# Kernel tuning notes

Hardware: AMD Instinct MI355X
Metric: run time of the kernel (lower is better)

The kernel has to match this reference:

```python
import jax, jax.numpy as jnp
import numpy as np

B, C, H, W = 32, 256, 64, 64
h, w = 8, 8          # partition size
S = 4                # num_sharesets
RED = 4              # globalperceptron_reduce
EPS = 1e-5           # BatchNorm eps


def setup_inputs() -> dict:
    key = jax.random.key(0)
    ks = jax.random.split(key, 20)
    Ci = C // RED
    def bn_params(i):
        return (1.0 + 0.1 * jax.random.normal(ks[i], (S,), jnp.float32),      # gamma
                0.1 * jax.random.normal(ks[i + 1], (S,), jnp.float32),        # beta
                0.1 * jax.random.normal(ks[i + 2], (S,), jnp.float32),        # running_mean
                jax.random.uniform(ks[i + 3], (S,), jnp.float32, 0.5, 1.5))   # running_var
    g3, b3, m3, v3 = bn_params(6)
    g1, b1, m1, v1 = bn_params(10)
    gk, bk, mk, vk = bn_params(14)
    return {
        "x": jax.random.normal(ks[0], (B, C, H, W), jnp.float32),
        # GlobalPerceptron (1x1 convs on pooled vector == dense layers)
        "fc1_w": 0.05 * jax.random.normal(ks[1], (Ci, C), jnp.float32),
        "fc1_b": jnp.zeros((Ci,), jnp.float32),
        "fc2_w": 0.05 * jax.random.normal(ks[2], (C, Ci), jnp.float32),
        "fc2_b": jnp.zeros((C,), jnp.float32),
        # fc3: grouped 1x1 conv over S*h*w channels -> S independent (h*w,h*w) mats
        "fc3_w": 0.05 * jax.random.normal(ks[3], (S, h * w, h * w), jnp.float32),
        "fc3bn_g": g3, "fc3bn_b": b3, "fc3bn_m": m3, "fc3bn_v": v3,
        # reparam depthwise conv branches (k=1 and k=3), groups=S
        "conv1_w": 0.1 * jax.random.normal(ks[4], (S, 1, 1, 1), jnp.float32),
        "bn1_g": g1, "bn1_b": b1, "bn1_m": m1, "bn1_v": v1,
        "conv3_w": 0.1 * jax.random.normal(ks[5], (S, 1, 3, 3), jnp.float32),
        "bn3_g": gk, "bn3_b": bk, "bn3_m": mk, "bn3_v": vk,
    }


def _bn(x, g, b, m, v):
    # inference-mode BatchNorm2d over channel dim 1 (S channels)
    scale = g / jnp.sqrt(v + EPS)
    return x * scale[None, :, None, None] + (b - m * scale)[None, :, None, None]


def _dwconv(x, wgt, k):
    # depthwise (groups=S) conv, stride 1, SAME-ish padding k//2
    return jax.lax.conv_general_dilated(
        x, wgt, (1, 1), [(k // 2, k // 2)] * 2,
        feature_group_count=S, dimension_numbers=("NCHW", "OIHW", "NCHW"))


def reference(x, fc1_w, fc1_b, fc2_w, fc2_b, fc3_w,
              fc3bn_g, fc3bn_b, fc3bn_m, fc3bn_v,
              conv1_w, bn1_g, bn1_b, bn1_m, bn1_v,
              conv3_w, bn3_g, bn3_b, bn3_m, bn3_v):
    hp, wp = H // h, W // w
    # GlobalPerceptron gate: avgpool -> fc -> relu -> fc -> sigmoid
    pooled = x.mean((2, 3))  # (B, C)
    gate = jax.nn.sigmoid(jnp.maximum(pooled @ fc1_w.T + fc1_b, 0.0) @ fc2_w.T + fc2_b)
    # partition: (B,C,H,W) -> (B,hp,wp,C,h,w)
    parts = x.reshape(B, C, hp, h, wp, w).transpose(0, 2, 4, 1, 3, 5)
    # fc3 grouped 1x1 conv: rows of S consecutive channels' (h*w) patches
    fc_in = parts.reshape(-1, S, h * w)                      # (B*hp*wp*C/S, S, h*w)
    fc3_out = jnp.einsum('nsi,soi->nso', fc_in, fc3_w).reshape(-1, S, h, w)
    fc3_out = _bn(fc3_out, fc3bn_g, fc3bn_b, fc3bn_m, fc3bn_v)
    # multi-branch depthwise convs on the same partitions, summed
    conv_in = parts.reshape(-1, S, h, w)
    conv_out = (_bn(_dwconv(conv_in, conv1_w, 1), bn1_g, bn1_b, bn1_m, bn1_v)
                + _bn(_dwconv(conv_in, conv3_w, 3), bn3_g, bn3_b, bn3_m, bn3_v))
    # merge, un-partition (literal translation of the torch reshape/permute chain)
    out = (fc3_out + conv_out).reshape(-1, hp, wp, S, h, w)
    out = out.transpose(0, 3, 1, 4, 2, 5).reshape(B, C, H, W)
    return out * gate[:, :, None, None]
```

## Files before the change

### kernel.cpp

```cpp
#include <hip/hip_runtime.h>
#include <hip/hip_bf16.h>
#include <math.h>

#define BN_EPS 1e-5f

typedef __attribute__((ext_vector_type(8))) short short8;
typedef __attribute__((ext_vector_type(4))) float f32x4;

__device__ __forceinline__ unsigned short bfbits(float f) {
  __hip_bfloat16 h = __float2bfloat16(f);
  return *reinterpret_cast<unsigned short*>(&h);
}
__device__ __forceinline__ float bf2f(unsigned short u) {
  union { unsigned v; float f; } c; c.v = ((unsigned)u) << 16;
  return c.f;
}

__global__ __launch_bounds__(256) void prep_pool_kernel(
    const float* __restrict__ x, float* __restrict__ pooled,
    const float* __restrict__ fc3_w,
    const float* __restrict__ g3, const float* __restrict__ b3,
    const float* __restrict__ m3, const float* __restrict__ v3,
    const float* __restrict__ c1w,
    const float* __restrict__ g1, const float* __restrict__ b1,
    const float* __restrict__ m1, const float* __restrict__ v1,
    const float* __restrict__ c3w,
    const float* __restrict__ gk, const float* __restrict__ bk,
    const float* __restrict__ mk, const float* __restrict__ vk,
    unsigned short* __restrict__ ahi, unsigned short* __restrict__ alo,
    float* __restrict__ totb) {
  int bid = blockIdx.x;
  int tid = threadIdx.x;
  if (bid < 16) {
    int s = bid >> 2;
    int o = (bid & 3) * 16 + (tid >> 4);
    int kc = (tid & 15) * 4;
    float sc3 = g3[s] * rsqrtf(v3[s] + BN_EPS);
    float sc1 = g1[s] * rsqrtf(v1[s] + BN_EPS);
    float sck = gk[s] * rsqrtf(vk[s] + BN_EPS);
    float c0 = sc1 * c1w[s] + sck * c3w[s * 9 + 4];
    int oh = o >> 3, ow = o & 7;
    unsigned short H[4], L[4];
#pragma unroll
    for (int j = 0; j < 4; ++j) {
      int k = kc + j;
      int kh = k >> 3, kw = k & 7;
      float a = sc3 * fc3_w[(s * 64 + o) * 64 + k];
      int dy = kh - oh, dx = kw - ow;
      if (dy >= -1 && dy <= 1 && dx >= -1 && dx <= 1)
        a += (dy == 0 && dx == 0) ? c0 : sck * c3w[s * 9 + (dy + 1) * 3 + (dx + 1)];
      unsigned short h = bfbits(a);
      H[j] = h;
      L[j] = bfbits(a - bf2f(h));
    }
    size_t base = (size_t)(s * 64 + o) * 64 + kc;
    *(ushort4*)(ahi + base) = make_ushort4(H[0], H[1], H[2], H[3]);
    *(ushort4*)(alo + base) = make_ushort4(L[0], L[1], L[2], L[3]);
    if (bid == 0 && tid < 4) {
      int ss = tid;
      float s3 = g3[ss] * rsqrtf(v3[ss] + BN_EPS);
      float s1 = g1[ss] * rsqrtf(v1[ss] + BN_EPS);
      float sk = gk[ss] * rsqrtf(vk[ss] + BN_EPS);
      totb[ss] = (b3[ss] - m3[ss] * s3) + (b1[ss] - m1[ss] * s1) + (bk[ss] - mk[ss] * sk);
    }
    return;
  }
  int w = tid >> 6, lane = tid & 63;
  int bc = (bid - 16) * 4 + w;
  const f32x4* xp = (const f32x4*)(x + (size_t)bc * 4096);
  float ssum = 0.f;
#pragma unroll
  for (int i = 0; i < 16; ++i) {
    f32x4 v = xp[i * 64 + lane];
    ssum += (v.x + v.y) + (v.z + v.w);
  }
#pragma unroll
  for (int m = 32; m >= 1; m >>= 1) ssum += __shfl_xor(ssum, m, 64);
  if (lane == 0) pooled[bc] = ssum * (1.f / 4096.f);
}

__global__ __launch_bounds__(256) void gate_kernel(const float* __restrict__ pooled,
                                                   const float* __restrict__ fc1_w,
                                                   const float* __restrict__ fc1_b,
                                                   const float* __restrict__ fc2_w,
                                                   const float* __restrict__ fc2_b,
                                                   float* __restrict__ gate) {
  int b = blockIdx.x;
  int tid = threadIdx.x;
  __shared__ float p[256];
  __shared__ float hbuf[64];
  p[tid] = pooled[b * 256 + tid];
  __syncthreads();
  if (tid < 64) {
    float a = fc1_b[tid];
    const float* wr = fc1_w + tid * 256;
#pragma unroll 8
    for (int c = 0; c < 256; ++c) a += p[c] * wr[c];
    hbuf[tid] = fmaxf(a, 0.f);
  }
  __syncthreads();
  float g = fc2_b[tid];
  const float* w2 = fc2_w + tid * 64;
#pragma unroll 8
  for (int j = 0; j < 64; ++j) g += hbuf[j] * w2[j];
  gate[b * 256 + tid] = 1.f / (1.f + expf(-g));
}

__global__ __launch_bounds__(512, 4) void main_kernel(
    const float* __restrict__ x,
    const unsigned short* __restrict__ ahi, const unsigned short* __restrict__ alo,
    const float* __restrict__ totb, const float* __restrict__ gate,
    float* __restrict__ out) {
  __shared__ unsigned short xs[33280];

  int bid = blockIdx.x;
  int cgh = bid & 7;
  int hpi = (bid >> 3) & 7;
  int b   = bid >> 6;
  int tid = threadIdx.x;
  int wv  = tid >> 6;
  int s    = __builtin_amdgcn_readfirstlane(wv & 3);
  int half = __builtin_amdgcn_readfirstlane(wv >> 2);
  int r16 = tid & 15;
  int g   = (tid >> 4) & 3;

  f32x4 gbuf[8];
#pragma unroll
  for (int i = 0; i < 8; ++i) {
    int flat = i * 512 + tid;
    int slot = flat >> 7;
    int off  = flat & 127;
    int row  = off >> 4, w4 = off & 15;
    int c = cgh * 32 + (slot & 7) * 4 + (slot >> 3);
    gbuf[i] = *(const f32x4*)(x + (size_t)(b * 256 + c) * 4096 + (hpi * 8 + row) * 64 + w4 * 4);
  }

  short8 Ah[2][2], Al[2][2];
#pragma unroll
  for (int oti = 0; oti < 2; ++oti)
#pragma unroll
    for (int kt = 0; kt < 2; ++kt) {
      size_t off = (size_t)(s * 64 + (half * 2 + oti) * 16 + r16) * 64 + kt * 32 + g * 8;
      Ah[kt][oti] = *(const short8*)(ahi + off);
      Al[kt][oti] = *(const short8*)(alo + off);
    }
  float gmul[4];
#pragma unroll
  for (int nt = 0; nt < 4; ++nt)
    gmul[nt] = gate[b * 256 + hpi * 32 + (nt * 2 + (r16 >> 3)) * 4 + s];
  float tb = totb[s];

#pragma unroll
  for (int i = 0; i < 8; ++i) {
    int flat = i * 512 + tid;
    int slot = flat >> 7;
    int off  = flat & 127;
    int row  = off >> 4, w4 = off & 15;
    float fv[4] = {gbuf[i].x, gbuf[i].y, gbuf[i].z, gbuf[i].w};
    ushort4 H, L;
    unsigned short h0 = bfbits(fv[0]), h1 = bfbits(fv[1]), h2 = bfbits(fv[2]), h3 = bfbits(fv[3]);
    H = make_ushort4(h0, h1, h2, h3);
    L = make_ushort4(bfbits(fv[0] - bf2f(h0)), bfbits(fv[1] - bf2f(h1)),
                     bfbits(fv[2] - bf2f(h2)), bfbits(fv[3] - bf2f(h3)));
    int base = slot * 520 + row * 64 + w4 * 4;
    *(ushort4*)&xs[base] = H;
    *(ushort4*)&xs[16640 + base] = L;
  }

  __syncthreads();

  f32x4 acc[2][4];
#pragma unroll
  for (int i = 0; i < 2; ++i)
#pragma unroll
    for (int j = 0; j < 4; ++j) acc[i][j] = f32x4{0.f, 0.f, 0.f, 0.f};

  int jch = r16 & 7;
#pragma unroll
  for (int kt = 0; kt < 2; ++kt)
#pragma unroll
    for (int nt = 0; nt < 4; ++nt) {
      int wpi = nt * 2 + (r16 >> 3);
      int addr = (s * 8 + jch) * 520 + (kt * 4 + g) * 64 + wpi * 8;
      short8 BH = *(const short8*)&xs[addr];
      short8 BL = *(const short8*)&xs[16640 + addr];
#pragma unroll
      for (int oti = 0; oti < 2; ++oti) {
        acc[oti][nt] = __builtin_amdgcn_mfma_f32_16x16x32_bf16(Ah[kt][oti], BH, acc[oti][nt], 0, 0, 0);
        acc[oti][nt] = __builtin_amdgcn_mfma_f32_16x16x32_bf16(Ah[kt][oti], BL, acc[oti][nt], 0, 0, 0);
        acc[oti][nt] = __builtin_amdgcn_mfma_f32_16x16x32_bf16(Al[kt][oti], BH, acc[oti][nt], 0, 0, 0);
      }
    }

#pragma unroll
  for (int nt = 0; nt < 4; ++nt) {
    int n2 = nt * 16 + r16;
    int c_out = hpi * 32 + (n2 >> 3) * 4 + s;
    float gm = gmul[nt];
    float* outb = out + (size_t)(b * 256 + c_out) * 4096 + cgh * 8 * 64 + (n2 & 7) * 8;
#pragma unroll
    for (int oti = 0; oti < 2; ++oti) {
      f32x4 a = acc[oti][nt];
      int hh = (half * 2 + oti) * 2 + (g >> 1);
      int wo = (g & 1) * 4;
      f32x4 o4 = {(a.x + tb) * gm, (a.y + tb) * gm,
                  (a.z + tb) * gm, (a.w + tb) * gm};
      __builtin_nontemporal_store(o4, (f32x4*)(outb + hh * 64 + wo));
    }
  }
}

extern "C" void kernel_launch(void* const* d_in, const int* in_sizes, int n_in,
                              void* d_out, int out_size, void* d_ws, size_t ws_size,
                              hipStream_t stream) {
  const float* x     = (const float*)d_in[0];
  const float* fc1_w = (const float*)d_in[1];
  const float* fc1_b = (const float*)d_in[2];
  const float* fc2_w = (const float*)d_in[3];
  const float* fc2_b = (const float*)d_in[4];
  const float* fc3_w = (const float*)d_in[5];
  const float* g3  = (const float*)d_in[6];
  const float* b3  = (const float*)d_in[7];
  const float* m3  = (const float*)d_in[8];
  const float* v3  = (const float*)d_in[9];
  const float* c1w = (const float*)d_in[10];
  const float* g1  = (const float*)d_in[11];
  const float* b1  = (const float*)d_in[12];
  const float* m1  = (const float*)d_in[13];
  const float* v1  = (const float*)d_in[14];
  const float* c3w = (const float*)d_in[15];
  const float* gk  = (const float*)d_in[16];
  const float* bk  = (const float*)d_in[17];
  const float* mk  = (const float*)d_in[18];
  const float* vk  = (const float*)d_in[19];
  float* out = (float*)d_out;

  float* pooled = (float*)d_ws;
  float* gate   = pooled + 8192;
  unsigned short* ahi = (unsigned short*)(gate + 8192);
  unsigned short* alo = ahi + 16384;
  float* totb   = (float*)(alo + 16384);

  prep_pool_kernel<<<2064, 256, 0, stream>>>(x, pooled, fc3_w, g3, b3, m3, v3,
                                             c1w, g1, b1, m1, v1, c3w, gk, bk,
                                             mk, vk, ahi, alo, totb);
  gate_kernel<<<32, 256, 0, stream>>>(pooled, fc1_w, fc1_b, fc2_w, fc2_b, gate);
  main_kernel<<<2048, 512, 0, stream>>>(x, ahi, alo, totb, gate, out);
}
```

Baseline: 75.20 us.

## Fuse gate MLP into main kernel and reverse block order

```diff
diff --git a/kernel.cpp b/kernel.cpp
--- a/kernel.cpp
+++ b/kernel.cpp
@@ -79,46 +79,25 @@
   if (lane == 0) pooled[bc] = ssum * (1.f / 4096.f);
 }
 
-__global__ __launch_bounds__(256) void gate_kernel(const float* __restrict__ pooled,
-                                                   const float* __restrict__ fc1_w,
-                                                   const float* __restrict__ fc1_b,
-                                                   const float* __restrict__ fc2_w,
-                                                   const float* __restrict__ fc2_b,
-                                                   float* __restrict__ gate) {
-  int b = blockIdx.x;
-  int tid = threadIdx.x;
-  __shared__ float p[256];
-  __shared__ float hbuf[64];
-  p[tid] = pooled[b * 256 + tid];
-  __syncthreads();
-  if (tid < 64) {
-    float a = fc1_b[tid];
-    const float* wr = fc1_w + tid * 256;
-#pragma unroll 8
-    for (int c = 0; c < 256; ++c) a += p[c] * wr[c];
-    hbuf[tid] = fmaxf(a, 0.f);
-  }
-  __syncthreads();
-  float g = fc2_b[tid];
-  const float* w2 = fc2_w + tid * 64;
-#pragma unroll 8
-  for (int j = 0; j < 64; ++j) g += hbuf[j] * w2[j];
-  gate[b * 256 + tid] = 1.f / (1.f + expf(-g));
-}
-
 __global__ __launch_bounds__(512, 4) void main_kernel(
     const float* __restrict__ x,
     const unsigned short* __restrict__ ahi, const unsigned short* __restrict__ alo,
-    const float* __restrict__ totb, const float* __restrict__ gate,
+    const float* __restrict__ totb, const float* __restrict__ pooled,
+    const float* __restrict__ fc1_w, const float* __restrict__ fc1_b,
+    const float* __restrict__ fc2_w, const float* __restrict__ fc2_b,
     float* __restrict__ out) {
   __shared__ unsigned short xs[33280];
-
-  int bid = blockIdx.x;
+  __shared__ float partL[512];
+  __shared__ float hidL[64];
+  __shared__ float gmulL[32];
+
+  int bid = 2047 - (int)blockIdx.x;
   int cgh = bid & 7;
   int hpi = (bid >> 3) & 7;
   int b   = bid >> 6;
   int tid = threadIdx.x;
   int wv  = tid >> 6;
+  int lane = tid & 63;
   int s    = __builtin_amdgcn_readfirstlane(wv & 3);
   int half = __builtin_amdgcn_readfirstlane(wv >> 2);
   int r16 = tid & 15;
@@ -135,6 +114,21 @@
     gbuf[i] = *(const f32x4*)(x + (size_t)(b * 256 + c) * 4096 + (hpi * 8 + row) * 64 + w4 * 4);
   }
 
+  {
+    int h = wv * 8 + (lane >> 3);
+    int k = lane & 7;
+    const float* fw = fc1_w + h * 256 + k * 32;
+    const float* pp = pooled + b * 256 + k * 32;
+    float pacc = 0.f;
+#pragma unroll
+    for (int j = 0; j < 8; ++j) {
+      f32x4 w4 = *(const f32x4*)(fw + j * 4);
+      f32x4 p4 = *(const f32x4*)(pp + j * 4);
+      pacc += w4.x * p4.x + w4.y * p4.y + w4.z * p4.z + w4.w * p4.w;
+    }
+    partL[k * 64 + h] = pacc;
+  }
+
   short8 Ah[2][2], Al[2][2];
 #pragma unroll
   for (int oti = 0; oti < 2; ++oti)
@@ -144,10 +138,6 @@
       Ah[kt][oti] = *(const short8*)(ahi + off);
       Al[kt][oti] = *(const short8*)(alo + off);
     }
-  float gmul[4];
-#pragma unroll
-  for (int nt = 0; nt < 4; ++nt)
-    gmul[nt] = gate[b * 256 + hpi * 32 + (nt * 2 + (r16 >> 3)) * 4 + s];
   float tb = totb[s];
 
 #pragma unroll
@@ -157,17 +147,35 @@
     int off  = flat & 127;
     int row  = off >> 4, w4 = off & 15;
     float fv[4] = {gbuf[i].x, gbuf[i].y, gbuf[i].z, gbuf[i].w};
-    ushort4 H, L;
     unsigned short h0 = bfbits(fv[0]), h1 = bfbits(fv[1]), h2 = bfbits(fv[2]), h3 = bfbits(fv[3]);
-    H = make_ushort4(h0, h1, h2, h3);
-    L = make_ushort4(bfbits(fv[0] - bf2f(h0)), bfbits(fv[1] - bf2f(h1)),
-                     bfbits(fv[2] - bf2f(h2)), bfbits(fv[3] - bf2f(h3)));
+    ushort4 H = make_ushort4(h0, h1, h2, h3);
+    ushort4 L = make_ushort4(bfbits(fv[0] - bf2f(h0)), bfbits(fv[1] - bf2f(h1)),
+                             bfbits(fv[2] - bf2f(h2)), bfbits(fv[3] - bf2f(h3)));
     int base = slot * 520 + row * 64 + w4 * 4;
     *(ushort4*)&xs[base] = H;
     *(ushort4*)&xs[16640 + base] = L;
   }
 
   __syncthreads();
+
+  if (wv == 0) {
+    float hsum = fc1_b[lane];
+#pragma unroll
+    for (int k2 = 0; k2 < 8; ++k2) hsum += partL[k2 * 64 + lane];
+    hidL[lane] = fmaxf(hsum, 0.f);
+    int r = lane >> 1, hf = lane & 1;
+    const float* w2 = fc2_w + (hpi * 32 + r) * 64 + hf * 32;
+    float p = 0.f;
+#pragma unroll
+    for (int j = 0; j < 32; j += 4) {
+      f32x4 w4 = *(const f32x4*)(w2 + j);
+      p += w4.x * hidL[hf * 32 + j] + w4.y * hidL[hf * 32 + j + 1]
+         + w4.z * hidL[hf * 32 + j + 2] + w4.w * hidL[hf * 32 + j + 3];
+    }
+    p += __shfl_xor(p, 1, 64);
+    float gv = 1.f / (1.f + expf(-(p + fc2_b[hpi * 32 + r])));
+    if (hf == 0) gmulL[r] = gv;
+  }
 
   f32x4 acc[2][4];
 #pragma unroll
@@ -192,11 +200,13 @@
       }
     }
 
+  __syncthreads();
+
 #pragma unroll
   for (int nt = 0; nt < 4; ++nt) {
     int n2 = nt * 16 + r16;
     int c_out = hpi * 32 + (n2 >> 3) * 4 + s;
-    float gm = gmul[nt];
+    float gm = gmulL[(nt * 2 + (r16 >> 3)) * 4 + s];
     float* outb = out + (size_t)(b * 256 + c_out) * 4096 + cgh * 8 * 64 + (n2 & 7) * 8;
 #pragma unroll
     for (int oti = 0; oti < 2; ++oti) {
@@ -236,14 +246,13 @@
   float* out = (float*)d_out;
 
   float* pooled = (float*)d_ws;
-  float* gate   = pooled + 8192;
-  unsigned short* ahi = (unsigned short*)(gate + 8192);
+  unsigned short* ahi = (unsigned short*)(pooled + 8192);
   unsigned short* alo = ahi + 16384;
   float* totb   = (float*)(alo + 16384);
 
   prep_pool_kernel<<<2064, 256, 0, stream>>>(x, pooled, fc3_w, g3, b3, m3, v3,
                                              c1w, g1, b1, m1, v1, c3w, gk, bk,
                                              mk, vk, ahi, alo, totb);
-  gate_kernel<<<32, 256, 0, stream>>>(pooled, fc1_w, fc1_b, fc2_w, fc2_b, gate);
-  main_kernel<<<2048, 512, 0, stream>>>(x, ahi, alo, totb, gate, out);
-}
+  main_kernel<<<2048, 512, 0, stream>>>(x, ahi, alo, totb, pooled,
+                                        fc1_w, fc1_b, fc2_w, fc2_b, out);
+}
```

Result: slower. 85.15 us (+13.2%).
